# Performance work log

Hardware: AMD Instinct MI355X
Metric: run time of the kernel (lower is better)

Reference implementation:

```python
import jax, jax.numpy as jnp
import numpy as np

B, N, C = 8, 16384, 40
E, KD, VD = 512, 256, 256


def setup_inputs() -> dict:
    key = jax.random.key(0)
    ks = jax.random.split(key, 10)
    s = 0.02
    return {
        "q": jax.random.normal(ks[0], (B, N, E), jnp.float32),
        "k": jax.random.normal(ks[1], (B, C, KD), jnp.float32),
        "v": jax.random.normal(ks[2], (B, C, VD), jnp.float32),
        "coarse_pred": jax.random.normal(ks[3], (B, C, N), jnp.float32),
        "Wq": jax.random.normal(ks[4], (E, E), jnp.float32) * s,
        "bq": jnp.zeros((E,), jnp.float32),
        "Wk": jax.random.normal(ks[5], (E, KD), jnp.float32) * s,
        "bk": jnp.zeros((E,), jnp.float32),
        "Wv": jax.random.normal(ks[6], (E, VD), jnp.float32) * s,
        "bv": jnp.zeros((E,), jnp.float32),
    }


def reference(q, k, v, coarse_pred, Wq, bq, Wk, bk, Wv, bv):
    # Projections (nn.Linear: x @ W.T + b)
    qp = jnp.einsum("bne,fe->bnf", q, Wq) + bq          # (B, N, E)
    kp = jnp.einsum("bcd,fd->bcf", k, Wk) + bk          # (B, C, E)
    vp = jnp.einsum("bcd,fd->bcf", v, Wv) + bv          # (B, C, E)

    scale = 1.0 / jnp.sqrt(jnp.float32(E))
    attn = jnp.einsum("bne,bce->bnc", qp, kp) * scale   # (B, N, C)
    attn = jax.nn.softmax(attn, axis=-1)

    # coarse_pred is detached, transposed to (B, N, C), softmaxed over classes
    cp = jax.nn.softmax(jnp.swapaxes(coarse_pred, 1, 2), axis=-1)
    attn = jax.nn.softmax(attn * cp, axis=-1)

    out = jnp.einsum("bnc,bce->bne", attn, vp)          # (B, N, E)
    return out
```

## Files before the change

### kernel.cpp

```cpp
#include <hip/hip_runtime.h>
#include <stdint.h>

#define Bb 8
#define Nn 16384
#define Cc 40
#define Ee 512
#define Dd 256

typedef __attribute__((ext_vector_type(4))) float f32x4;
typedef __attribute__((ext_vector_type(8))) short bf16x8;

__device__ __forceinline__ unsigned short f2bf(float f) {
  union { float f; uint32_t u; } x; x.f = f;
  uint32_t r = x.u + 0x7FFFu + ((x.u >> 16) & 1u);
  return (unsigned short)(r >> 16);
}
__device__ __forceinline__ unsigned int pack2(float a, float b) {
  return (unsigned int)f2bf(a) | ((unsigned int)f2bf(b) << 16);
}

__global__ __launch_bounds__(256) void prep0_kernel(
    const float* __restrict__ Wq, const float* __restrict__ Wk,
    float* __restrict__ Mt) {
  __shared__ float WqL[64][68];
  __shared__ float WkL[64][68];
  const int t = threadIdx.x;
  const int te = (t & 15) * 4;
  const int td = (t >> 4) * 4;
  const int ebase = blockIdx.x * 64, dbase = blockIdx.y * 64;
  const int fbase = blockIdx.z * 256;
  f32x4 acc0 = {0,0,0,0}, acc1 = {0,0,0,0}, acc2 = {0,0,0,0}, acc3 = {0,0,0,0};
  for (int f0 = 0; f0 < 256; f0 += 64) {
    __syncthreads();
    #pragma unroll
    for (int i = 0; i < 4; i++) {
      int idx = t + i * 256;
      int row = idx >> 4, c4 = (idx & 15) * 4;
      *(float4*)&WqL[row][c4] = *(const float4*)(Wq + (size_t)(fbase + f0 + row) * Ee + ebase + c4);
      *(float4*)&WkL[row][c4] = *(const float4*)(Wk + (size_t)(fbase + f0 + row) * Dd + dbase + c4);
    }
    __syncthreads();
    #pragma unroll 8
    for (int ff = 0; ff < 64; ff++) {
      float4 a = *(const float4*)&WkL[ff][td];
      float4 b = *(const float4*)&WqL[ff][te];
      acc0[0] += a.x*b.x; acc0[1] += a.x*b.y; acc0[2] += a.x*b.z; acc0[3] += a.x*b.w;
      acc1[0] += a.y*b.x; acc1[1] += a.y*b.y; acc1[2] += a.y*b.z; acc1[3] += a.y*b.w;
      acc2[0] += a.z*b.x; acc2[1] += a.z*b.y; acc2[2] += a.z*b.z; acc2[3] += a.z*b.w;
      acc3[0] += a.w*b.x; acc3[1] += a.w*b.y; acc3[2] += a.w*b.z; acc3[3] += a.w*b.w;
    }
  }
  float* mt = Mt + (size_t)blockIdx.z * 131072;
  *(f32x4*)&mt[(size_t)(dbase + td + 0) * Ee + ebase + te] = acc0;
  *(f32x4*)&mt[(size_t)(dbase + td + 1) * Ee + ebase + te] = acc1;
  *(f32x4*)&mt[(size_t)(dbase + td + 2) * Ee + ebase + te] = acc2;
  *(f32x4*)&mt[(size_t)(dbase + td + 3) * Ee + ebase + te] = acc3;
}

__global__ __launch_bounds__(256) void prep0b_kernel(
    const float* __restrict__ Wq, const float* __restrict__ Wk,
    const float* __restrict__ bq, const float* __restrict__ bk,
    float* __restrict__ tvec, float* __restrict__ uvec, float* __restrict__ bqbk) {
  const int t = threadIdx.x, bx = blockIdx.x;
  if (bx < 2) {
    const int e = bx * 256 + t;
    float s = 0.f;
    #pragma unroll 8
    for (int f = 0; f < Ee; f++) s += Wq[(size_t)f * Ee + e] * bk[f];
    tvec[e] = s;
  } else {
    const int d = t;
    float s = 0.f;
    #pragma unroll 8
    for (int f = 0; f < Ee; f++) s += Wk[(size_t)f * Dd + d] * bq[f];
    uvec[d] = s;
    __shared__ float red[256];
    float p = 0.f;
    for (int f = t; f < Ee; f += 256) p += bq[f] * bk[f];
    red[t] = p; __syncthreads();
    #pragma unroll
    for (int off = 128; off > 0; off >>= 1) {
      if (t < off) red[t] += red[t + off];
      __syncthreads();
    }
    if (t == 0) bqbk[0] = red[0];
  }
}

__global__ __launch_bounds__(256) void prep1_kernel(
    const float* __restrict__ k, const float* __restrict__ Mt,
    const float* __restrict__ tvec, const float* __restrict__ uvec,
    const float* __restrict__ bqbk, unsigned short* __restrict__ abf,
    float* __restrict__ dbias) {
  __shared__ float kL[8][Dd];
  const int t = threadIdx.x;
  const int el = t & 127, half = t >> 7;
  const int e = blockIdx.y * 128 + el;
  const int sbase = blockIdx.x * 8;
  for (int i = t; i < 8 * Dd; i += 256) {
    int row = i >> 8, dd = i & (Dd - 1);
    int sg = sbase + row, bb_ = sg / 48, cc = sg % 48;
    kL[row][dd] = (cc < 40) ? k[((size_t)bb_ * Cc + cc) * Dd + dd] : 0.f;
  }
  __syncthreads();
  float acc[4] = {0,0,0,0};
  float db[4]  = {0,0,0,0};
  #pragma unroll 4
  for (int d = 0; d < Dd; d++) {
    float mt = Mt[(size_t)d * Ee + e] + Mt[131072 + (size_t)d * Ee + e];
    float ud = uvec[d];
    #pragma unroll
    for (int si = 0; si < 4; si++) {
      float kv = kL[half*4 + si][d];
      acc[si] += mt * kv;
      db[si]  += ud * kv;
    }
  }
  const float scale = 0.044194173824159216f;
  const float te = tvec[e];
  const float bqbkv = bqbk[0];
  const int ks = e >> 5, gg = (e >> 3) & 3, j = e & 7;
  #pragma unroll
  for (int si = 0; si < 4; si++) {
    int sg = sbase + half*4 + si, bb_ = sg / 48, cc = sg % 48;
    int ct = cc >> 4, lane16 = (cc & 15) + 16*gg;
    unsigned short val = (cc < 40) ? f2bf(scale * (acc[si] + te)) : (unsigned short)0;
    abf[((((size_t)bb_*3 + ct)*16 + ks)*64 + lane16)*8 + j] = val;
    if (el == 0) dbias[bb_*64 + cc] = (cc < 40) ? scale * (db[si] + bqbkv) : 0.f;
  }
}

__global__ __launch_bounds__(256) void prep2_kernel(
    const float* __restrict__ v, const float* __restrict__ Wv,
    const float* __restrict__ bv, unsigned short* __restrict__ vpf) {
  __shared__ float vL[8][Dd];
  const int t = threadIdx.x;
  const int el = t & 127, half = t >> 7;
  const int e = blockIdx.y * 128 + el;
  const int sbase = blockIdx.x * 8;
  for (int i = t; i < 8 * Dd; i += 256) {
    int row = i >> 8, dd = i & (Dd - 1);
    int sg = sbase + row, bb_ = sg >> 6, cc = sg & 63;
    vL[row][dd] = (cc < 40) ? v[((size_t)bb_ * Cc + cc) * Dd + dd] : 0.f;
  }
  __syncthreads();
  const float* wrow = Wv + (size_t)e * Dd;
  float acc[4] = {0,0,0,0};
  #pragma unroll 2
  for (int dd = 0; dd < Dd; dd += 4) {
    float4 w = *(const float4*)(wrow + dd);
    #pragma unroll
    for (int si = 0; si < 4; si++) {
      float4 vv = *(const float4*)&vL[half*4 + si][dd];
      acc[si] += w.x*vv.x + w.y*vv.y + w.z*vv.z + w.w*vv.w;
    }
  }
  const float bve = bv[e];
  const int nt = e >> 4, elan = e & 15;
  #pragma unroll
  for (int si = 0; si < 4; si++) {
    int sg = sbase + half*4 + si, bb_ = sg >> 6, cc = sg & 63;
    int s = cc >> 5, gg = (cc >> 3) & 3, j = cc & 7;
    unsigned short val = (cc < 40) ? f2bf(acc[si] + bve) : (unsigned short)0;
    vpf[((((size_t)bb_*32 + nt)*2 + s)*64 + (elan + 16*gg))*8 + j] = val;
  }
}

__global__ __launch_bounds__(256, 3) void main_kernel(
    const float* __restrict__ q, const float* __restrict__ coarse,
    const unsigned short* __restrict__ abfrag,
    const unsigned short* __restrict__ vpfrag,
    const float* __restrict__ dbias, float* __restrict__ out) {
  __shared__ float4 s_q[4][2][256];
  __shared__ unsigned short s_att[4][16][72];
  const int t = threadIdx.x;
  const int wave = t >> 6, lane = t & 63;
  const int r = lane & 15, g = lane >> 4;
  const int bid = blockIdx.x;
  const int b = bid >> 8, nb = bid & 255;
  const int nw = nb * 64 + wave * 16;

  const int sr0 = lane >> 4;
  const int scolb = (lane & 15) << 4;
  const int swzA = scolb ^ (sr0 << 4);
  const float* qstage = q + (size_t)(b * Nn + nw + sr0) * Ee + ((lane & 15) << 2);
  char* const qb0 = (char*)&s_q[wave][0][0];
  char* const qb1 = (char*)&s_q[wave][1][0];
  const int wo0 = sr0*256 + 0*1024 + swzA;
  const int wo1 = sr0*256 + 1*1024 + (swzA ^ 0x40);
  const int wo2 = sr0*256 + 2*1024 + swzA;
  const int wo3 = sr0*256 + 3*1024 + (swzA ^ 0x40);
  const int rbase = r * 256;
  const int rswz = (r & 7) << 4;

  const bf16x8* abf = (const bf16x8*)abfrag + (size_t)b * 3 * 16 * 64 + lane;

  f32x4 acc0 = {0,0,0,0}, acc1 = {0,0,0,0}, acc2 = {0,0,0,0};
  float4 S0[4], S1[4];

  auto LOADC = [&](int c, float4* S) {
    #pragma unroll
    for (int j = 0; j < 4; j++)
      S[j] = *(const float4*)(qstage + (size_t)4*j*Ee + c*64);
  };
  auto DSW = [&](float4* S, char* qb) {
    *(float4*)(qb + wo0) = S[0];
    *(float4*)(qb + wo1) = S[1];
    *(float4*)(qb + wo2) = S[2];
    *(float4*)(qb + wo3) = S[3];
  };
  auto COMP = [&](int c, char* qb) {
    #pragma unroll
    for (int ksl = 0; ksl < 2; ksl++) {
      const int x = 128*ksl + 32*g;
      float4 qa = *(const float4*)(qb + rbase + ((x     ) ^ rswz));
      float4 qc = *(const float4*)(qb + rbase + ((x + 16) ^ rswz));
      bf16x8 qf;
      qf[0]=(short)f2bf(qa.x); qf[1]=(short)f2bf(qa.y);
      qf[2]=(short)f2bf(qa.z); qf[3]=(short)f2bf(qa.w);
      qf[4]=(short)f2bf(qc.x); qf[5]=(short)f2bf(qc.y);
      qf[6]=(short)f2bf(qc.z); qf[7]=(short)f2bf(qc.w);
      const int ks = 2*c + ksl;
      acc0 = __builtin_amdgcn_mfma_f32_16x16x32_bf16(abf[(0*16+ks)*64], qf, acc0, 0,0,0);
      acc1 = __builtin_amdgcn_mfma_f32_16x16x32_bf16(abf[(1*16+ks)*64], qf, acc1, 0,0,0);
      acc2 = __builtin_amdgcn_mfma_f32_16x16x32_bf16(abf[(2*16+ks)*64], qf, acc2, 0,0,0);
    }
  };

  LOADC(0, S0); LOADC(1, S1); DSW(S0, qb0);
  LOADC(2, S0); COMP(0, qb0); DSW(S1, qb1);
  LOADC(3, S1); COMP(1, qb1); DSW(S0, qb0);
  LOADC(4, S0); COMP(2, qb0); DSW(S1, qb1);
  LOADC(5, S1); COMP(3, qb1); DSW(S0, qb0);
  LOADC(6, S0); COMP(4, qb0); DSW(S1, qb1);
  LOADC(7, S1); COMP(5, qb1); DSW(S0, qb0);
                COMP(6, qb0); DSW(S1, qb1);
                COMP(7, qb1);

  float L[3][4];
  #pragma unroll
  for (int rg = 0; rg < 4; rg++) {
    L[0][rg] = acc0[rg] + dbias[b*64 +  0 + 4*g + rg];
    L[1][rg] = acc1[rg] + dbias[b*64 + 16 + 4*g + rg];
    L[2][rg] = acc2[rg] + dbias[b*64 + 32 + 4*g + rg];
  }
  const bool v2 = (g < 2);

  float m1 = -3e38f;
  #pragma unroll
  for (int rg = 0; rg < 4; rg++) {
    m1 = fmaxf(m1, L[0][rg]); m1 = fmaxf(m1, L[1][rg]);
    if (v2) m1 = fmaxf(m1, L[2][rg]);
  }
  m1 = fmaxf(m1, __shfl_xor(m1, 16));
  m1 = fmaxf(m1, __shfl_xor(m1, 32));
  float p[3][4]; float s1 = 0.f;
  #pragma unroll
  for (int rg = 0; rg < 4; rg++) {
    p[0][rg] = __expf(L[0][rg] - m1); s1 += p[0][rg];
    p[1][rg] = __expf(L[1][rg] - m1); s1 += p[1][rg];
    p[2][rg] = v2 ? __expf(L[2][rg] - m1) : 0.f; s1 += p[2][rg];
  }
  s1 += __shfl_xor(s1, 16); s1 += __shfl_xor(s1, 32);
  const float inv1 = 1.0f / s1;

  const float* cbase = coarse + (size_t)b * Cc * Nn + (nw + r);
  float cr[3][4];
  #pragma unroll
  for (int rg = 0; rg < 4; rg++) {
    cr[0][rg] = cbase[(size_t)( 0 + 4*g + rg) * Nn];
    cr[1][rg] = cbase[(size_t)(16 + 4*g + rg) * Nn];
    cr[2][rg] = v2 ? cbase[(size_t)(32 + 4*g + rg) * Nn] : -3e38f;
  }
  float m2 = -3e38f;
  #pragma unroll
  for (int rg = 0; rg < 4; rg++) {
    m2 = fmaxf(m2, cr[0][rg]); m2 = fmaxf(m2, cr[1][rg]);
    if (v2) m2 = fmaxf(m2, cr[2][rg]);
  }
  m2 = fmaxf(m2, __shfl_xor(m2, 16));
  m2 = fmaxf(m2, __shfl_xor(m2, 32));
  float cpv[3][4]; float s2 = 0.f;
  #pragma unroll
  for (int rg = 0; rg < 4; rg++) {
    cpv[0][rg] = __expf(cr[0][rg] - m2); s2 += cpv[0][rg];
    cpv[1][rg] = __expf(cr[1][rg] - m2); s2 += cpv[1][rg];
    cpv[2][rg] = v2 ? __expf(cr[2][rg] - m2) : 0.f; s2 += cpv[2][rg];
  }
  s2 += __shfl_xor(s2, 16); s2 += __shfl_xor(s2, 32);
  const float inv2 = 1.0f / s2;

  const float sc12 = inv1 * inv2;
  float w[3][4];
  float m3 = -3e38f;
  #pragma unroll
  for (int rg = 0; rg < 4; rg++) {
    w[0][rg] = p[0][rg] * cpv[0][rg] * sc12;
    w[1][rg] = p[1][rg] * cpv[1][rg] * sc12;
    w[2][rg] = v2 ? (p[2][rg] * cpv[2][rg] * sc12) : 0.f;
    m3 = fmaxf(m3, w[0][rg]); m3 = fmaxf(m3, w[1][rg]);
    if (v2) m3 = fmaxf(m3, w[2][rg]);
  }
  m3 = fmaxf(m3, __shfl_xor(m3, 16));
  m3 = fmaxf(m3, __shfl_xor(m3, 32));
  float p3[3][4]; float s3 = 0.f;
  #pragma unroll
  for (int rg = 0; rg < 4; rg++) {
    p3[0][rg] = __expf(w[0][rg] - m3); s3 += p3[0][rg];
    p3[1][rg] = __expf(w[1][rg] - m3); s3 += p3[1][rg];
    p3[2][rg] = v2 ? __expf(w[2][rg] - m3) : 0.f; s3 += p3[2][rg];
  }
  s3 += __shfl_xor(s3, 16); s3 += __shfl_xor(s3, 32);
  const float inv3 = 1.0f / s3;

  unsigned int* srow = (unsigned int*)&s_att[wave][r][0];
  #pragma unroll
  for (int ct = 0; ct < 3; ct++) {
    srow[8*ct + 2*g + 0] = pack2(p3[ct][0]*inv3, p3[ct][1]*inv3);
    srow[8*ct + 2*g + 1] = pack2(p3[ct][2]*inv3, p3[ct][3]*inv3);
  }
  srow[24 + 2*g + 0] = 0u;
  srow[24 + 2*g + 1] = 0u;
  asm volatile("s_waitcnt lgkmcnt(0)" ::: "memory");
  const bf16x8 pa0 = *(const bf16x8*)&s_att[wave][r][ 0 + 8*g];
  const bf16x8 pa1 = *(const bf16x8*)&s_att[wave][r][32 + 8*g];

  const bf16x8* vpf = (const bf16x8*)vpfrag + (size_t)b * 32 * 2 * 64 + lane;
  float* outb = out + ((size_t)b * Nn + nw) * Ee;
  #pragma unroll 8
  for (int nt = 0; nt < 32; nt++) {
    bf16x8 vf0 = vpf[(nt*2 + 0)*64];
    bf16x8 vf1 = vpf[(nt*2 + 1)*64];
    f32x4 o = {0,0,0,0};
    o = __builtin_amdgcn_mfma_f32_16x16x32_bf16(pa0, vf0, o, 0,0,0);
    o = __builtin_amdgcn_mfma_f32_16x16x32_bf16(pa1, vf1, o, 0,0,0);
    #pragma unroll
    for (int rg = 0; rg < 4; rg++)
      outb[(size_t)(4*g + rg) * Ee + nt*16 + r] = o[rg];
  }
}

extern "C" void kernel_launch(void* const* d_in, const int* in_sizes, int n_in,
                              void* d_out, int out_size, void* d_ws, size_t ws_size,
                              hipStream_t stream) {
  const float* q   = (const float*)d_in[0];
  const float* k   = (const float*)d_in[1];
  const float* v   = (const float*)d_in[2];
  const float* cps = (const float*)d_in[3];
  const float* Wq  = (const float*)d_in[4];
  const float* bq  = (const float*)d_in[5];
  const float* Wk  = (const float*)d_in[6];
  const float* bk  = (const float*)d_in[7];
  const float* Wv  = (const float*)d_in[8];
  const float* bv  = (const float*)d_in[9];
  float* out = (float*)d_out;
  char* ws = (char*)d_ws;

  float*          Mt    = (float*)(ws);
  float*          tvec  = (float*)(ws + 1048576);
  float*          uvec  = (float*)(ws + 1050624);
  float*          bqbkp = (float*)(ws + 1051648);
  unsigned short* abf   = (unsigned short*)(ws + 1052672);
  unsigned short* vpf   = (unsigned short*)(ws + 1052672 + 393216);
  float*          dbias = (float*)(ws + 1052672 + 393216 + 524288);

  prep0_kernel <<<dim3(8, 4, 2), 256, 0, stream>>>(Wq, Wk, Mt);
  prep0b_kernel<<<dim3(3),       256, 0, stream>>>(Wq, Wk, bq, bk, tvec, uvec, bqbkp);
  prep2_kernel <<<dim3(64, 4),   256, 0, stream>>>(v, Wv, bv, vpf);
  prep1_kernel <<<dim3(48, 4),   256, 0, stream>>>(k, Mt, tvec, uvec, bqbkp, abf, dbias);
  main_kernel  <<<dim3(2048),    256, 0, stream>>>(q, cps, abf, vpf, dbias, out);
}
```

Measured before the change: 215.7 us.

## Merge prep kernels and make main kernel single-wave with direct register Q loads

Merges the four prep kernels into two launches by folding the bias-vector computations into the Mt GEMM grid and combining the k and v projections into one grid. The main kernel becomes one 64-thread wave per block. Each lane loads its Q fragments straight from global memory into registers with double buffering, which drops the swizzled LDS staging. The coarse_pred and dbias loads are hoisted ahead of the GEMM to hide their latency. The trade-offs are much higher register pressure, less coalesced Q loads, and four times as many tiny blocks.

```diff
diff --git a/kernel.cpp b/kernel.cpp
--- a/kernel.cpp
+++ b/kernel.cpp
@@ -19,12 +19,43 @@
   return (unsigned int)f2bf(a) | ((unsigned int)f2bf(b) << 16);
 }
 
-__global__ __launch_bounds__(256) void prep0_kernel(
+__global__ __launch_bounds__(256) void prepA_kernel(
     const float* __restrict__ Wq, const float* __restrict__ Wk,
-    float* __restrict__ Mt) {
+    const float* __restrict__ bq, const float* __restrict__ bk,
+    float* __restrict__ Mt, float* __restrict__ tvec,
+    float* __restrict__ uvec, float* __restrict__ bqbk) {
+  const int t = threadIdx.x;
+  if (blockIdx.x == 8) {
+    if (blockIdx.z != 0) return;
+    const int by = blockIdx.y;
+    if (by < 2) {
+      const int e = by * 256 + t;
+      float s = 0.f;
+      #pragma unroll 8
+      for (int f = 0; f < Ee; f++) s += Wq[(size_t)f * Ee + e] * bk[f];
+      tvec[e] = s;
+    } else if (by == 2) {
+      const int d = t;
+      float s = 0.f;
+      #pragma unroll 8
+      for (int f = 0; f < Ee; f++) s += Wk[(size_t)f * Dd + d] * bq[f];
+      uvec[d] = s;
+    } else {
+      __shared__ float red[256];
+      float p = 0.f;
+      for (int f = t; f < Ee; f += 256) p += bq[f] * bk[f];
+      red[t] = p; __syncthreads();
+      #pragma unroll
+      for (int off = 128; off > 0; off >>= 1) {
+        if (t < off) red[t] += red[t + off];
+        __syncthreads();
+      }
+      if (t == 0) bqbk[0] = red[0];
+    }
+    return;
+  }
   __shared__ float WqL[64][68];
   __shared__ float WkL[64][68];
-  const int t = threadIdx.x;
   const int te = (t & 15) * 4;
   const int td = (t >> 4) * 4;
   const int ebase = blockIdx.x * 64, dbase = blockIdx.y * 64;
@@ -57,194 +88,161 @@
   *(f32x4*)&mt[(size_t)(dbase + td + 3) * Ee + ebase + te] = acc3;
 }
 
-__global__ __launch_bounds__(256) void prep0b_kernel(
-    const float* __restrict__ Wq, const float* __restrict__ Wk,
-    const float* __restrict__ bq, const float* __restrict__ bk,
-    float* __restrict__ tvec, float* __restrict__ uvec, float* __restrict__ bqbk) {
-  const int t = threadIdx.x, bx = blockIdx.x;
-  if (bx < 2) {
-    const int e = bx * 256 + t;
-    float s = 0.f;
-    #pragma unroll 8
-    for (int f = 0; f < Ee; f++) s += Wq[(size_t)f * Ee + e] * bk[f];
-    tvec[e] = s;
-  } else {
-    const int d = t;
-    float s = 0.f;
-    #pragma unroll 8
-    for (int f = 0; f < Ee; f++) s += Wk[(size_t)f * Dd + d] * bq[f];
-    uvec[d] = s;
-    __shared__ float red[256];
-    float p = 0.f;
-    for (int f = t; f < Ee; f += 256) p += bq[f] * bk[f];
-    red[t] = p; __syncthreads();
-    #pragma unroll
-    for (int off = 128; off > 0; off >>= 1) {
-      if (t < off) red[t] += red[t + off];
-      __syncthreads();
-    }
-    if (t == 0) bqbk[0] = red[0];
-  }
-}
-
-__global__ __launch_bounds__(256) void prep1_kernel(
-    const float* __restrict__ k, const float* __restrict__ Mt,
-    const float* __restrict__ tvec, const float* __restrict__ uvec,
-    const float* __restrict__ bqbk, unsigned short* __restrict__ abf,
+__global__ __launch_bounds__(256) void prepB_kernel(
+    const float* __restrict__ k, const float* __restrict__ v,
+    const float* __restrict__ Wv, const float* __restrict__ bv,
+    const float* __restrict__ Mt, const float* __restrict__ tvec,
+    const float* __restrict__ uvec, const float* __restrict__ bqbk,
+    unsigned short* __restrict__ abf, unsigned short* __restrict__ vpf,
     float* __restrict__ dbias) {
-  __shared__ float kL[8][Dd];
+  __shared__ float xL[8][Dd];
   const int t = threadIdx.x;
   const int el = t & 127, half = t >> 7;
   const int e = blockIdx.y * 128 + el;
-  const int sbase = blockIdx.x * 8;
-  for (int i = t; i < 8 * Dd; i += 256) {
-    int row = i >> 8, dd = i & (Dd - 1);
-    int sg = sbase + row, bb_ = sg / 48, cc = sg % 48;
-    kL[row][dd] = (cc < 40) ? k[((size_t)bb_ * Cc + cc) * Dd + dd] : 0.f;
-  }
-  __syncthreads();
-  float acc[4] = {0,0,0,0};
-  float db[4]  = {0,0,0,0};
-  #pragma unroll 4
-  for (int d = 0; d < Dd; d++) {
-    float mt = Mt[(size_t)d * Ee + e] + Mt[131072 + (size_t)d * Ee + e];
-    float ud = uvec[d];
+
+  if (blockIdx.x < 48) {
+    const int sbase = blockIdx.x * 8;
+    for (int i = t; i < 8 * Dd; i += 256) {
+      int row = i >> 8, dd = i & (Dd - 1);
+      int sg = sbase + row, bb_ = sg / 48, cc = sg % 48;
+      xL[row][dd] = (cc < 40) ? k[((size_t)bb_ * Cc + cc) * Dd + dd] : 0.f;
+    }
+    __syncthreads();
+    float acc[4] = {0,0,0,0};
+    float db[4]  = {0,0,0,0};
+    #pragma unroll 4
+    for (int d = 0; d < Dd; d++) {
+      float mt = Mt[(size_t)d * Ee + e] + Mt[131072 + (size_t)d * Ee + e];
+      float ud = uvec[d];
+      #pragma unroll
+      for (int si = 0; si < 4; si++) {
+        float kv = xL[half*4 + si][d];
+        acc[si] += mt * kv;
+        db[si]  += ud * kv;
+      }
+    }
+    const float scale = 0.044194173824159216f;
+    const float te = tvec[e];
+    const float bqbkv = bqbk[0];
+    const int ks = e >> 5, gg = (e >> 3) & 3, j = e & 7;
     #pragma unroll
     for (int si = 0; si < 4; si++) {
-      float kv = kL[half*4 + si][d];
-      acc[si] += mt * kv;
-      db[si]  += ud * kv;
-    }
-  }
-  const float scale = 0.044194173824159216f;
-  const float te = tvec[e];
-  const float bqbkv = bqbk[0];
-  const int ks = e >> 5, gg = (e >> 3) & 3, j = e & 7;
-  #pragma unroll
-  for (int si = 0; si < 4; si++) {
-    int sg = sbase + half*4 + si, bb_ = sg / 48, cc = sg % 48;
-    int ct = cc >> 4, lane16 = (cc & 15) + 16*gg;
-    unsigned short val = (cc < 40) ? f2bf(scale * (acc[si] + te)) : (unsigned short)0;
-    abf[((((size_t)bb_*3 + ct)*16 + ks)*64 + lane16)*8 + j] = val;
-    if (el == 0) dbias[bb_*64 + cc] = (cc < 40) ? scale * (db[si] + bqbkv) : 0.f;
-  }
-}
-
-__global__ __launch_bounds__(256) void prep2_kernel(
-    const float* __restrict__ v, const float* __restrict__ Wv,
-    const float* __restrict__ bv, unsigned short* __restrict__ vpf) {
-  __shared__ float vL[8][Dd];
-  const int t = threadIdx.x;
-  const int el = t & 127, half = t >> 7;
-  const int e = blockIdx.y * 128 + el;
-  const int sbase = blockIdx.x * 8;
-  for (int i = t; i < 8 * Dd; i += 256) {
-    int row = i >> 8, dd = i & (Dd - 1);
-    int sg = sbase + row, bb_ = sg >> 6, cc = sg & 63;
-    vL[row][dd] = (cc < 40) ? v[((size_t)bb_ * Cc + cc) * Dd + dd] : 0.f;
-  }
-  __syncthreads();
-  const float* wrow = Wv + (size_t)e * Dd;
-  float acc[4] = {0,0,0,0};
-  #pragma unroll 2
-  for (int dd = 0; dd < Dd; dd += 4) {
-    float4 w = *(const float4*)(wrow + dd);
+      int sg = sbase + half*4 + si, bb_ = sg / 48, cc = sg % 48;
+      int ct = cc >> 4, lane16 = (cc & 15) + 16*gg;
+      unsigned short val = (cc < 40) ? f2bf(scale * (acc[si] + te)) : (unsigned short)0;
+      abf[((((size_t)bb_*3 + ct)*16 + ks)*64 + lane16)*8 + j] = val;
+      if (el == 0) dbias[bb_*64 + cc] = (cc < 40) ? scale * (db[si] + bqbkv) : 0.f;
+    }
+  } else {
+    const int sbase = (blockIdx.x - 48) * 8;
+    for (int i = t; i < 8 * Dd; i += 256) {
+      int row = i >> 8, dd = i & (Dd - 1);
+      int sg = sbase + row, bb_ = sg >> 6, cc = sg & 63;
+      xL[row][dd] = (cc < 40) ? v[((size_t)bb_ * Cc + cc) * Dd + dd] : 0.f;
+    }
+    __syncthreads();
+    const float* wrow = Wv + (size_t)e * Dd;
+    float acc[4] = {0,0,0,0};
+    #pragma unroll 2
+    for (int dd = 0; dd < Dd; dd += 4) {
+      float4 w = *(const float4*)(wrow + dd);
+      #pragma unroll
+      for (int si = 0; si < 4; si++) {
+        float4 vv = *(const float4*)&xL[half*4 + si][dd];
+        acc[si] += w.x*vv.x + w.y*vv.y + w.z*vv.z + w.w*vv.w;
+      }
+    }
+    const float bve = bv[e];
+    const int nt = e >> 4, elan = e & 15;
     #pragma unroll
     for (int si = 0; si < 4; si++) {
-      float4 vv = *(const float4*)&vL[half*4 + si][dd];
-      acc[si] += w.x*vv.x + w.y*vv.y + w.z*vv.z + w.w*vv.w;
-    }
-  }
-  const float bve = bv[e];
-  const int nt = e >> 4, elan = e & 15;
-  #pragma unroll
-  for (int si = 0; si < 4; si++) {
-    int sg = sbase + half*4 + si, bb_ = sg >> 6, cc = sg & 63;
-    int s = cc >> 5, gg = (cc >> 3) & 3, j = cc & 7;
-    unsigned short val = (cc < 40) ? f2bf(acc[si] + bve) : (unsigned short)0;
-    vpf[((((size_t)bb_*32 + nt)*2 + s)*64 + (elan + 16*gg))*8 + j] = val;
-  }
-}
-
-__global__ __launch_bounds__(256, 3) void main_kernel(
+      int sg = sbase + half*4 + si, bb_ = sg >> 6, cc = sg & 63;
+      int s = cc >> 5, gg = (cc >> 3) & 3, j = cc & 7;
+      unsigned short val = (cc < 40) ? f2bf(acc[si] + bve) : (unsigned short)0;
+      vpf[((((size_t)bb_*32 + nt)*2 + s)*64 + (elan + 16*gg))*8 + j] = val;
+    }
+  }
+}
+
+__global__ __launch_bounds__(64, 4) void main_kernel(
     const float* __restrict__ q, const float* __restrict__ coarse,
     const unsigned short* __restrict__ abfrag,
     const unsigned short* __restrict__ vpfrag,
     const float* __restrict__ dbias, float* __restrict__ out) {
-  __shared__ float4 s_q[4][2][256];
-  __shared__ unsigned short s_att[4][16][72];
-  const int t = threadIdx.x;
-  const int wave = t >> 6, lane = t & 63;
+  __shared__ unsigned short s_att[16][72];
+  const int lane = threadIdx.x;
   const int r = lane & 15, g = lane >> 4;
   const int bid = blockIdx.x;
-  const int b = bid >> 8, nb = bid & 255;
-  const int nw = nb * 64 + wave * 16;
-
-  const int sr0 = lane >> 4;
-  const int scolb = (lane & 15) << 4;
-  const int swzA = scolb ^ (sr0 << 4);
-  const float* qstage = q + (size_t)(b * Nn + nw + sr0) * Ee + ((lane & 15) << 2);
-  char* const qb0 = (char*)&s_q[wave][0][0];
-  char* const qb1 = (char*)&s_q[wave][1][0];
-  const int wo0 = sr0*256 + 0*1024 + swzA;
-  const int wo1 = sr0*256 + 1*1024 + (swzA ^ 0x40);
-  const int wo2 = sr0*256 + 2*1024 + swzA;
-  const int wo3 = sr0*256 + 3*1024 + (swzA ^ 0x40);
-  const int rbase = r * 256;
-  const int rswz = (r & 7) << 4;
-
+  const int b = bid >> 10;
+  const int nw = (bid & 1023) << 4;
+  const float* qrow = q + ((size_t)b * Nn + nw + r) * Ee + 8 * g;
   const bf16x8* abf = (const bf16x8*)abfrag + (size_t)b * 3 * 16 * 64 + lane;
+  const bool v2 = (g < 2);
 
   f32x4 acc0 = {0,0,0,0}, acc1 = {0,0,0,0}, acc2 = {0,0,0,0};
-  float4 S0[4], S1[4];
-
-  auto LOADC = [&](int c, float4* S) {
-    #pragma unroll
-    for (int j = 0; j < 4; j++)
-      S[j] = *(const float4*)(qstage + (size_t)4*j*Ee + c*64);
-  };
-  auto DSW = [&](float4* S, char* qb) {
-    *(float4*)(qb + wo0) = S[0];
-    *(float4*)(qb + wo1) = S[1];
-    *(float4*)(qb + wo2) = S[2];
-    *(float4*)(qb + wo3) = S[3];
-  };
-  auto COMP = [&](int c, char* qb) {
-    #pragma unroll
-    for (int ksl = 0; ksl < 2; ksl++) {
-      const int x = 128*ksl + 32*g;
-      float4 qa = *(const float4*)(qb + rbase + ((x     ) ^ rswz));
-      float4 qc = *(const float4*)(qb + rbase + ((x + 16) ^ rswz));
+  float4 A0[8], A1[8];
+
+  #pragma unroll
+  for (int j = 0; j < 4; j++) {
+    A0[2*j]   = *(const float4*)(qrow + 32*j);
+    A0[2*j+1] = *(const float4*)(qrow + 32*j + 4);
+  }
+  #pragma unroll
+  for (int j = 0; j < 4; j++) {
+    A1[2*j]   = *(const float4*)(qrow + 128 + 32*j);
+    A1[2*j+1] = *(const float4*)(qrow + 128 + 32*j + 4);
+  }
+
+  const float* cbase = coarse + (size_t)b * Cc * Nn + (nw + r);
+  float cr[3][4];
+  #pragma unroll
+  for (int rg = 0; rg < 4; rg++) {
+    cr[0][rg] = cbase[(size_t)( 0 + 4*g + rg) * Nn];
+    cr[1][rg] = cbase[(size_t)(16 + 4*g + rg) * Nn];
+    cr[2][rg] = v2 ? cbase[(size_t)(32 + 4*g + rg) * Nn] : -3e38f;
+  }
+  float4 db0 = *(const float4*)(dbias + b*64 +  0 + 4*g);
+  float4 db1 = *(const float4*)(dbias + b*64 + 16 + 4*g);
+  float4 db2 = *(const float4*)(dbias + b*64 + 32 + 4*g);
+
+  auto COMP = [&](const float4* A, int c) {
+    #pragma unroll
+    for (int j = 0; j < 4; j++) {
+      float4 qa = A[2*j], qc = A[2*j+1];
       bf16x8 qf;
       qf[0]=(short)f2bf(qa.x); qf[1]=(short)f2bf(qa.y);
       qf[2]=(short)f2bf(qa.z); qf[3]=(short)f2bf(qa.w);
       qf[4]=(short)f2bf(qc.x); qf[5]=(short)f2bf(qc.y);
       qf[6]=(short)f2bf(qc.z); qf[7]=(short)f2bf(qc.w);
-      const int ks = 2*c + ksl;
+      const int ks = 4*c + j;
       acc0 = __builtin_amdgcn_mfma_f32_16x16x32_bf16(abf[(0*16+ks)*64], qf, acc0, 0,0,0);
       acc1 = __builtin_amdgcn_mfma_f32_16x16x32_bf16(abf[(1*16+ks)*64], qf, acc1, 0,0,0);
       acc2 = __builtin_amdgcn_mfma_f32_16x16x32_bf16(abf[(2*16+ks)*64], qf, acc2, 0,0,0);
     }
   };
 
-  LOADC(0, S0); LOADC(1, S1); DSW(S0, qb0);
-  LOADC(2, S0); COMP(0, qb0); DSW(S1, qb1);
-  LOADC(3, S1); COMP(1, qb1); DSW(S0, qb0);
-  LOADC(4, S0); COMP(2, qb0); DSW(S1, qb1);
-  LOADC(5, S1); COMP(3, qb1); DSW(S0, qb0);
-  LOADC(6, S0); COMP(4, qb0); DSW(S1, qb1);
-  LOADC(7, S1); COMP(5, qb1); DSW(S0, qb0);
-                COMP(6, qb0); DSW(S1, qb1);
-                COMP(7, qb1);
+  COMP(A0, 0);
+  #pragma unroll
+  for (int j = 0; j < 4; j++) {
+    A0[2*j]   = *(const float4*)(qrow + 256 + 32*j);
+    A0[2*j+1] = *(const float4*)(qrow + 256 + 32*j + 4);
+  }
+  COMP(A1, 1);
+  #pragma unroll
+  for (int j = 0; j < 4; j++) {
+    A1[2*j]   = *(const float4*)(qrow + 384 + 32*j);
+    A1[2*j+1] = *(const float4*)(qrow + 384 + 32*j + 4);
+  }
+  COMP(A0, 2);
+  COMP(A1, 3);
 
   float L[3][4];
   #pragma unroll
   for (int rg = 0; rg < 4; rg++) {
-    L[0][rg] = acc0[rg] + dbias[b*64 +  0 + 4*g + rg];
-    L[1][rg] = acc1[rg] + dbias[b*64 + 16 + 4*g + rg];
-    L[2][rg] = acc2[rg] + dbias[b*64 + 32 + 4*g + rg];
-  }
-  const bool v2 = (g < 2);
+    L[0][rg] = acc0[rg] + ((const float*)&db0)[rg];
+    L[1][rg] = acc1[rg] + ((const float*)&db1)[rg];
+    L[2][rg] = acc2[rg] + ((const float*)&db2)[rg];
+  }
 
   float m1 = -3e38f;
   #pragma unroll
@@ -264,14 +262,6 @@
   s1 += __shfl_xor(s1, 16); s1 += __shfl_xor(s1, 32);
   const float inv1 = 1.0f / s1;
 
-  const float* cbase = coarse + (size_t)b * Cc * Nn + (nw + r);
-  float cr[3][4];
-  #pragma unroll
-  for (int rg = 0; rg < 4; rg++) {
-    cr[0][rg] = cbase[(size_t)( 0 + 4*g + rg) * Nn];
-    cr[1][rg] = cbase[(size_t)(16 + 4*g + rg) * Nn];
-    cr[2][rg] = v2 ? cbase[(size_t)(32 + 4*g + rg) * Nn] : -3e38f;
-  }
   float m2 = -3e38f;
   #pragma unroll
   for (int rg = 0; rg < 4; rg++) {
@@ -313,7 +303,7 @@
   s3 += __shfl_xor(s3, 16); s3 += __shfl_xor(s3, 32);
   const float inv3 = 1.0f / s3;
 
-  unsigned int* srow = (unsigned int*)&s_att[wave][r][0];
+  unsigned int* srow = (unsigned int*)&s_att[r][0];
   #pragma unroll
   for (int ct = 0; ct < 3; ct++) {
     srow[8*ct + 2*g + 0] = pack2(p3[ct][0]*inv3, p3[ct][1]*inv3);
@@ -322,8 +312,8 @@
   srow[24 + 2*g + 0] = 0u;
   srow[24 + 2*g + 1] = 0u;
   asm volatile("s_waitcnt lgkmcnt(0)" ::: "memory");
-  const bf16x8 pa0 = *(const bf16x8*)&s_att[wave][r][ 0 + 8*g];
-  const bf16x8 pa1 = *(const bf16x8*)&s_att[wave][r][32 + 8*g];
+  const bf16x8 pa0 = *(const bf16x8*)&s_att[r][ 0 + 8*g];
+  const bf16x8 pa1 = *(const bf16x8*)&s_att[r][32 + 8*g];
 
   const bf16x8* vpf = (const bf16x8*)vpfrag + (size_t)b * 32 * 2 * 64 + lane;
   float* outb = out + ((size_t)b * Nn + nw) * Ee;
@@ -364,9 +354,8 @@
   unsigned short* vpf   = (unsigned short*)(ws + 1052672 + 393216);
   float*          dbias = (float*)(ws + 1052672 + 393216 + 524288);
 
-  prep0_kernel <<<dim3(8, 4, 2), 256, 0, stream>>>(Wq, Wk, Mt);
-  prep0b_kernel<<<dim3(3),       256, 0, stream>>>(Wq, Wk, bq, bk, tvec, uvec, bqbkp);
-  prep2_kernel <<<dim3(64, 4),   256, 0, stream>>>(v, Wv, bv, vpf);
-  prep1_kernel <<<dim3(48, 4),   256, 0, stream>>>(k, Mt, tvec, uvec, bqbkp, abf, dbias);
-  main_kernel  <<<dim3(2048),    256, 0, stream>>>(q, cps, abf, vpf, dbias, out);
-}
+  prepA_kernel<<<dim3(9, 4, 2), 256, 0, stream>>>(Wq, Wk, bq, bk, Mt, tvec, uvec, bqbkp);
+  prepB_kernel<<<dim3(112, 4),  256, 0, stream>>>(k, v, Wv, bv, Mt, tvec, uvec, bqbkp,
+                                                  abf, vpf, dbias);
+  main_kernel <<<dim3(8192),     64, 0, stream>>>(q, cps, abf, vpf, dbias, out);
+}
```

Result: faster. 206.1 us (-4.4%).
